# Kernel tuning notes

Hardware: AMD Instinct MI355X
Metric: run time of the kernel (lower is better)

Reference implementation:

```python
import jax, jax.numpy as jnp
import numpy as np

EPS = 1e-5

def _offset_conv(x, w, b):
    # 3x3 conv, padding=1, producing 2*K*K offset channels (standard DeformConv2D v1)
    out = jax.lax.conv_general_dilated(x, w, (1, 1), ((1, 1), (1, 1)),
                                       dimension_numbers=('NCHW', 'OIHW', 'NCHW'))
    return out + b[None, :, None, None]

def _bilinear_gather(x, py, px):
    # x: [B,C,H,W]; py,px: [B,K2,H,W] float sample coords -> [B,C,K2,H,W]
    B, C, H, W = x.shape
    py = jnp.clip(py, 0.0, H - 1.0)
    px = jnp.clip(px, 0.0, W - 1.0)
    y0 = jnp.floor(py)
    x0 = jnp.floor(px)
    wy = py - y0
    wx = px - x0
    y0i = y0.astype(jnp.int32)
    x0i = x0.astype(jnp.int32)
    y1i = jnp.minimum(y0i + 1, H - 1)
    x1i = jnp.minimum(x0i + 1, W - 1)
    xf = x.reshape(B, C, H * W)
    K2, Ho, Wo = py.shape[1], py.shape[2], py.shape[3]
    def gather(yy, xx):
        idx = (yy * W + xx).reshape(B, 1, -1)  # broadcast over C
        return jnp.take_along_axis(xf, idx, axis=2).reshape(B, C, K2, Ho, Wo)
    v00 = gather(y0i, x0i)
    v01 = gather(y0i, x1i)
    v10 = gather(y1i, x0i)
    v11 = gather(y1i, x1i)
    wy = wy[:, None]
    wx = wx[:, None]
    return (v00 * (1 - wy) * (1 - wx) + v01 * (1 - wy) * wx
            + v10 * wy * (1 - wx) + v11 * wy * wx)

def _deform_dw(x, w_off, b_off, w_dw, k):
    # depthwise deformable conv, kernel k, padding k//2 (same spatial size)
    B, C, H, W = x.shape
    K2 = k * k
    off = _offset_conv(x, w_off, b_off)      # [B, 2*K2, H, W]
    dy, dx = off[:, :K2], off[:, K2:]
    r = (k - 1) // 2
    pn = jnp.arange(-r, r + 1, dtype=x.dtype)
    pn_y = jnp.repeat(pn, k)[None, :, None, None]  # [1,K2,1,1]
    pn_x = jnp.tile(pn, k)[None, :, None, None]
    gy = jnp.arange(H, dtype=x.dtype)[None, None, :, None]
    gx = jnp.arange(W, dtype=x.dtype)[None, None, None, :]
    py = gy + pn_y + dy
    px = gx + pn_x + dx
    samp = _bilinear_gather(x, py, px)        # [B,C,K2,H,W]
    return jnp.einsum('bckhw,ck->bchw', samp, w_dw.reshape(C, K2))

def _bn_relu(x, g, b, m, v):
    inv = g / jnp.sqrt(v + EPS)
    return jax.nn.relu(x * inv[None, :, None, None] + (b - m * inv)[None, :, None, None])

def setup_inputs() -> dict:
    key = jax.random.key(0)
    B, C, H, W, O = 4, 96, 64, 64, 192
    ks = jax.random.split(key, 32)
    d = {'x': jax.random.normal(ks[0], (B, C, H, W), jnp.float32)}
    i = 1
    for k in (3, 5, 7):
        K2 = k * k
        d[f'w_off{k}'] = 0.01 * jax.random.normal(ks[i], (2 * K2, C, 3, 3), jnp.float32); i += 1
        d[f'b_off{k}'] = jnp.zeros((2 * K2,), jnp.float32)
        d[f'w_dw{k}'] = jax.random.normal(ks[i], (C, k, k), jnp.float32) / k; i += 1
        d[f'g{k}'] = jnp.ones((C,), jnp.float32)
        d[f'be{k}'] = jnp.zeros((C,), jnp.float32)
        d[f'm{k}'] = 0.1 * jax.random.normal(ks[i], (C,), jnp.float32); i += 1
        d[f'v{k}'] = jax.random.uniform(ks[i], (C,), jnp.float32, 0.5, 1.5); i += 1
    d['w_pw'] = jax.random.normal(ks[i], (O, 3 * C), jnp.float32) / np.sqrt(3 * C).astype(np.float32); i += 1
    d['gp'] = jnp.ones((O,), jnp.float32)
    d['bp'] = jnp.zeros((O,), jnp.float32)
    d['mp'] = 0.1 * jax.random.normal(ks[i], (O,), jnp.float32); i += 1
    d['vp'] = jax.random.uniform(ks[i], (O,), jnp.float32, 0.5, 1.5)
    return d

def reference(x, w_off3, b_off3, w_dw3, g3, be3, m3, v3,
              w_off5, b_off5, w_dw5, g5, be5, m5, v5,
              w_off7, b_off7, w_dw7, g7, be7, m7, v7,
              w_pw, gp, bp, mp, vp):
    x1 = _bn_relu(_deform_dw(x, w_off3, b_off3, w_dw3, 3), g3, be3, m3, v3)
    x2 = _bn_relu(_deform_dw(x, w_off5, b_off5, w_dw5, 5), g5, be5, m5, v5)
    x3 = _bn_relu(_deform_dw(x, w_off7, b_off7, w_dw7, 7), g7, be7, m7, v7)
    xc = jnp.concatenate([x1, x2, x3], axis=1)  # [B, 3C, H, W]
    out = jnp.einsum('bchw,oc->bohw', xc, w_pw)  # 1x1 conv
    return _bn_relu(out, gp, bp, mp, vp)
```

## Files before the change

### kernel.cpp

```cpp
#include <hip/hip_runtime.h>
#include <hip/hip_fp16.h>
#include <math.h>

typedef unsigned short u16;
typedef _Float16 f16x8 __attribute__((ext_vector_type(8)));
typedef float f32x4 __attribute__((ext_vector_type(4)));

#define HWp 4096
#define Cc 96
#define Bb 4
#define Oo 192
#define C3 288

#define OFF_WDWT  0
#define OFF_BCAT  14112
#define OFF_SBR   14304
#define OFF_HBR   14592
#define OFF_SPW   14880
#define OFF_HPW   15072
#define FP32_END  15264
#define BF_XTPAD  0
#define BF_WOF    1672704
#define BF_WPW    1838592

__device__ __forceinline__ u16 f2h(float f) { return __half_as_ushort(__float2half(f)); }
__device__ __forceinline__ unsigned h2u(__half2 h) { union { __half2 h; unsigned u; } t; t.h = h; return t.u; }
__device__ __forceinline__ __half2 u2h(unsigned u) { union { __half2 h; unsigned u; } t; t.u = u; return t.h; }

#define PREP_N (165888 + 55296 + 14112 + 192 + 288 + 288 + 192 + 192 + 24960)
#define PREP_BLK ((PREP_N + 255) / 256)

__global__ __launch_bounds__(256) void prep_kernel(
    const float* __restrict__ x,
    const float* __restrict__ w3, const float* __restrict__ b3, const float* __restrict__ dw3,
    const float* __restrict__ g3, const float* __restrict__ be3, const float* __restrict__ m3, const float* __restrict__ v3,
    const float* __restrict__ w5, const float* __restrict__ b5, const float* __restrict__ dw5,
    const float* __restrict__ g5, const float* __restrict__ be5, const float* __restrict__ m5, const float* __restrict__ v5,
    const float* __restrict__ w7, const float* __restrict__ b7, const float* __restrict__ dw7,
    const float* __restrict__ g7, const float* __restrict__ be7, const float* __restrict__ m7, const float* __restrict__ v7,
    const float* __restrict__ wpw,
    const float* __restrict__ gp, const float* __restrict__ bp, const float* __restrict__ mp, const float* __restrict__ vp,
    float* __restrict__ ws)
{
    __shared__ u16 sT[64 * 104];
    u16* bf = (u16*)(ws + FP32_END);
    const int tid = threadIdx.x;

    if (blockIdx.x < 256) {
        const int b = blockIdx.x >> 6, h = blockIdx.x & 63;
        const float* xb = x + (((size_t)b * Cc) << 12) + (h << 6);
#pragma unroll
        for (int it = 0; it < 24; ++it) {
            int j = tid + it * 256;
            int c = j >> 6, p = j & 63;
            sT[p * 104 + c] = f2h(xb[((size_t)c << 12) + p]);
        }
        __syncthreads();
        u16* dst = bf + BF_XTPAD + ((size_t)(b * 66 + h + 1) * 66 + 1) * 96;
#pragma unroll
        for (int it = 0; it < 6; ++it) {
            int j = tid + it * 256;
            int pos = j / 24, c4 = j % 24;
            const u16* s = &sT[pos * 104 + c4 * 4];
            *(uint2*)(dst + pos * 96 + c4 * 4) = make_uint2(
                (unsigned)s[0] | ((unsigned)s[1] << 16),
                (unsigned)s[2] | ((unsigned)s[3] << 16));
        }
        return;
    }

    int i = (blockIdx.x - 256) * 256 + tid;
    if (i < 165888) {
        int f = i / 13824, r = i % 13824;
        int s = r >> 9, l = r & 511;
        int lane = l >> 3, j = l & 7;
        int o = f * 16 + (lane & 15);
        int k = s * 32 + (lane >> 4) * 8 + j;
        int tap = k / 96, c = k % 96;
        float v = 0.f;
        if (o < 18)       v = w3[o * 864 + c * 9 + tap];
        else if (o < 68)  v = w5[(o - 18) * 864 + c * 9 + tap];
        else if (o < 166) v = w7[(o - 68) * 864 + c * 9 + tap];
        bf[BF_WOF + i] = f2h(v);
        return;
    }
    int j = i - 165888;
    if (j < 55296) {
        int f = j / 4608, r = j % 4608;
        int s = r >> 9, l = r & 511;
        int lane = l >> 3, jj = l & 7;
        int o = f * 16 + (lane & 15);
        int k = s * 32 + (lane >> 4) * 8 + jj;
        bf[BF_WPW + j] = f2h(wpw[o * C3 + k]);
        return;
    }
    j -= 55296;
    if (j < 14112) {
        int ksel = j / 4704, rem = j % 4704;
        int t = rem / 96, c = rem % 96;
        int K2 = (ksel == 0) ? 9 : (ksel == 1) ? 25 : 49;
        const float* dw = (ksel == 0) ? dw3 : (ksel == 1) ? dw5 : dw7;
        ws[OFF_WDWT + j] = (t < K2) ? dw[c * K2 + t] : 0.f;
        return;
    }
    j -= 14112;
    if (j < 192) {
        float v = 0.f;
        if (j < 18)       v = b3[j];
        else if (j < 68)  v = b5[j - 18];
        else if (j < 166) v = b7[j - 68];
        ws[OFF_BCAT + j] = v;
        return;
    }
    j -= 192;
    if (j < C3) {
        int ks = j / Cc, c = j % Cc;
        const float* g = (ks == 0) ? g3 : (ks == 1) ? g5 : g7;
        const float* v = (ks == 0) ? v3 : (ks == 1) ? v5 : v7;
        ws[OFF_SBR + j] = g[c] / sqrtf(v[c] + 1e-5f);
        return;
    }
    j -= C3;
    if (j < C3) {
        int ks = j / Cc, c = j % Cc;
        const float* g = (ks == 0) ? g3 : (ks == 1) ? g5 : g7;
        const float* v = (ks == 0) ? v3 : (ks == 1) ? v5 : v7;
        const float* be = (ks == 0) ? be3 : (ks == 1) ? be5 : be7;
        const float* m = (ks == 0) ? m3 : (ks == 1) ? m5 : m7;
        float inv = g[c] / sqrtf(v[c] + 1e-5f);
        ws[OFF_HBR + j] = be[c] - m[c] * inv;
        return;
    }
    j -= C3;
    if (j < Oo) { ws[OFF_SPW + j] = gp[j] / sqrtf(vp[j] + 1e-5f); return; }
    j -= Oo;
    if (j < Oo) {
        float inv = gp[j] / sqrtf(vp[j] + 1e-5f);
        ws[OFF_HPW + j] = bp[j] - mp[j] * inv;
        return;
    }
    j -= Oo;
    if (j < 24960) {
        int c4 = j % 24, rem = j / 24;
        int cell = rem % 260, bb = rem / 260;
        int row, col;
        if (cell < 66)       { row = 0;  col = cell; }
        else if (cell < 132) { row = 65; col = cell - 66; }
        else if (cell < 196) { row = cell - 132 + 1; col = 0; }
        else                 { row = cell - 196 + 1; col = 65; }
        u16* dst = bf + BF_XTPAD + ((size_t)(bb * 66 + row) * 66 + col) * 96 + c4 * 4;
        *(uint2*)dst = make_uint2(0u, 0u);
        return;
    }
}

__global__ __launch_bounds__(256, 4) void mega_kernel(
    const float* __restrict__ ws, float* __restrict__ out)
{
    __shared__ __align__(16) unsigned char shA[15936];
    __shared__ float regB[3072];
    u16* sX = (u16*)shA;
    uint2* sWab = (uint2*)shA;
    unsigned* sPk = (unsigned*)(shA + 10624);
    float* soff = regB;
    u16* ytile = (u16*)regB;

    const u16* bf = (const u16*)(ws + FP32_END);
    const u16* xp = bf + BF_XTPAD;
    const int tid = threadIdx.x;
    const int lane = tid & 63, wid = tid >> 6;
    const int lane15 = lane & 15, quad = lane >> 4;

    const int bx = blockIdx.x;
    const int xcd = bx & 7;
    const int b = xcd >> 1;
    const int tile = ((bx >> 3) << 1) + (xcd & 1);
    const int p0 = tile * 16;
    const int h = p0 >> 6;
    const int w0 = p0 & 63;

    {
        const u16* src = xp + ((size_t)(b * 66 + h) * 66 + w0) * 96;
        for (int j = tid; j < 1296; j += 256) {
            int r = j / 432;
            int rem = j % 432;
            int col = rem / 24, c4 = rem % 24;
            uint2 v = *(const uint2*)(src + ((size_t)(r * 66 + col)) * 96 + c4 * 4);
            *(uint2*)(&sX[(r * 18 + col) * 104 + c4 * 4]) = v;
        }
    }
    __syncthreads();

    {
        const u16* wof = bf + BF_WOF;
        f32x4 acc[3];
#pragma unroll
        for (int ff = 0; ff < 3; ++ff) acc[ff] = (f32x4){0.f, 0.f, 0.f, 0.f};
#pragma unroll
        for (int tap = 0; tap < 9; ++tap) {
            const int ky2 = tap / 3, kx2 = tap % 3;
            const u16* brow = &sX[(ky2 * 18 + kx2 + lane15) * 104 + quad * 8];
#pragma unroll
            for (int cc = 0; cc < 3; ++cc) {
                f16x8 bb = *(const f16x8*)(brow + cc * 32);
                const int s = tap * 3 + cc;
#pragma unroll
                for (int ff = 0; ff < 3; ++ff) {
                    const int f = wid * 3 + ff;
                    f16x8 a = *(const f16x8*)(wof + ((size_t)(f * 27 + s) * 64 + lane) * 8);
                    acc[ff] = __builtin_amdgcn_mfma_f32_16x16x32_f16(a, bb, acc[ff], 0, 0, 0);
                }
            }
        }
        const float* bcat = ws + OFF_BCAT;
#pragma unroll
        for (int ff = 0; ff < 3; ++ff) {
#pragma unroll
            for (int r = 0; r < 4; ++r) {
                int co = (wid * 3 + ff) * 16 + quad * 4 + r;
                soff[co * 16 + lane15] = acc[ff][r] + bcat[co];
            }
        }
    }
    __syncthreads();

    for (int i = tid; i < 1328; i += 256) {
        int gt = i >> 4, q = i & 15;
        int K, K2, R, tb, t;
        if (gt < 9)       { K = 3; K2 = 9;  R = 1; tb = 0;  t = gt; }
        else if (gt < 34) { K = 5; K2 = 25; R = 2; tb = 18; t = gt - 9; }
        else              { K = 7; K2 = 49; R = 3; tb = 68; t = gt - 34; }
        int ky = t / K - R, kx = t % K - R;
        float dy = soff[(tb + t) * 16 + q];
        float dx = soff[(tb + K2 + t) * 16 + q];
        float py = fminf(fmaxf((float)(h + ky) + dy, 0.f), 63.f);
        float px = fminf(fmaxf((float)(w0 + q + kx) + dx, 0.f), 63.f);
        float fy = floorf(py), fx = floorf(px);
        int y0 = (int)fy, x0 = (int)fx;
        float wy = py - fy, wx = px - fx;
        int y1 = min(y0 + 1, 63), x1 = min(x0 + 1, 63);
        float w11 = wy * wx;
        float w10 = wy - w11;
        float w01 = wx - w11;
        float w00 = 1.f - wy - wx + w11;
        unsigned wA = h2u(__floats2half2_rn(w00, w01));
        unsigned wB = h2u(__floats2half2_rn(w10, w11));
        unsigned o00 = (unsigned)((y0 + 1) * 66 + (x0 + 1)) * 192u;
        sWab[i] = make_uint2(wA, wB);
        sPk[i] = o00 | ((unsigned)(x1 - x0) << 20) | ((unsigned)(y1 - y0) << 21);
    }
    __syncthreads();

    if (tid < 192) {
        const int c8 = tid % 12;
        const int q  = tid / 12;
        const int c = c8 * 8;
        const u16* xh = xp + (size_t)b * 66 * 66 * 96;
        const char* xcb = (const char*)xh + c * 2;

#pragma unroll
        for (int seg = 0; seg < 3; ++seg) {
            const int g0 = (seg == 0) ? 0 : (seg == 1) ? 9 : 34;
            const int g1 = (seg == 0) ? 9 : (seg == 1) ? 34 : 83;
            const float* wdT = ws + OFF_WDWT + seg * 4704 + c;
            float acc[8];
#pragma unroll
            for (int k = 0; k < 8; ++k) acc[k] = 0.f;

            for (int gt = g0; gt < g1; ++gt) {
                const uint2 wab = sWab[(gt << 4) + q];
                const unsigned pk = sPk[(gt << 4) + q];
                const __half2 wAh = u2h(wab.x), wBh = u2h(wab.y);
                const __half2 w00b = __low2half2(wAh), w01b = __high2half2(wAh);
                const __half2 w10b = __low2half2(wBh), w11b = __high2half2(wBh);
                const unsigned d01 = ((pk >> 20) & 1u) * 192u;
                const unsigned d10 = ((pk >> 21) & 1u) * 12672u;
                const char* pb = xcb + (pk & 0xFFFFFu);
                const uint4 u00 = *(const uint4*)(pb);
                const uint4 u01 = *(const uint4*)(pb + d01);
                const uint4 u10 = *(const uint4*)(pb + d10);
                const uint4 u11 = *(const uint4*)(pb + d10 + d01);
                const float4 wda = *(const float4*)(wdT + (gt - g0) * 96);
                const float4 wdb = *(const float4*)(wdT + (gt - g0) * 96 + 4);
                const unsigned a00[4] = {u00.x, u00.y, u00.z, u00.w};
                const unsigned a01[4] = {u01.x, u01.y, u01.z, u01.w};
                const unsigned a10[4] = {u10.x, u10.y, u10.z, u10.w};
                const unsigned a11[4] = {u11.x, u11.y, u11.z, u11.w};
                const float wd[8] = {wda.x, wda.y, wda.z, wda.w, wdb.x, wdb.y, wdb.z, wdb.w};
#pragma unroll
                for (int d = 0; d < 4; ++d) {
                    __half2 v = __hmul2(w00b, u2h(a00[d]));
                    v = __hfma2(w01b, u2h(a01[d]), v);
                    v = __hfma2(w10b, u2h(a10[d]), v);
                    v = __hfma2(w11b, u2h(a11[d]), v);
                    acc[2 * d]     = fmaf(wd[2 * d],     __low2float(v),  acc[2 * d]);
                    acc[2 * d + 1] = fmaf(wd[2 * d + 1], __high2float(v), acc[2 * d + 1]);
                }
            }

            const int cb = seg * Cc + c;
            const float4 sa = *(const float4*)(ws + OFF_SBR + cb);
            const float4 sb = *(const float4*)(ws + OFF_SBR + cb + 4);
            const float4 ha = *(const float4*)(ws + OFF_HBR + cb);
            const float4 hb = *(const float4*)(ws + OFF_HBR + cb + 4);
            const float ss[8] = {sa.x, sa.y, sa.z, sa.w, sb.x, sb.y, sb.z, sb.w};
            const float hh8[8] = {ha.x, ha.y, ha.z, ha.w, hb.x, hb.y, hb.z, hb.w};
            unsigned rr[4];
#pragma unroll
            for (int d = 0; d < 4; ++d) {
                float lo = fmaxf(fmaf(acc[2 * d],     ss[2 * d],     hh8[2 * d]),     0.f);
                float hi = fmaxf(fmaf(acc[2 * d + 1], ss[2 * d + 1], hh8[2 * d + 1]), 0.f);
                rr[d] = h2u(__floats2half2_rn(lo, hi));
            }
            *(uint4*)(ytile + q * 296 + cb) = make_uint4(rr[0], rr[1], rr[2], rr[3]);
        }
    }
    __syncthreads();

    {
        const u16* wpw = bf + BF_WPW;
        f32x4 acc[3];
#pragma unroll
        for (int ff = 0; ff < 3; ++ff) acc[ff] = (f32x4){0.f, 0.f, 0.f, 0.f};
        const u16* brow = &ytile[lane15 * 296 + quad * 8];
#pragma unroll
        for (int s = 0; s < 9; ++s) {
            f16x8 bb = *(const f16x8*)(brow + s * 32);
#pragma unroll
            for (int ff = 0; ff < 3; ++ff) {
                const int f = wid * 3 + ff;
                f16x8 a = *(const f16x8*)(wpw + ((size_t)(f * 9 + s) * 64 + lane) * 8);
                acc[ff] = __builtin_amdgcn_mfma_f32_16x16x32_f16(a, bb, acc[ff], 0, 0, 0);
            }
        }
        const float* spw = ws + OFF_SPW;
        const float* hpw = ws + OFF_HPW;
        const int p = p0 + lane15;
#pragma unroll
        for (int ff = 0; ff < 3; ++ff) {
#pragma unroll
            for (int r = 0; r < 4; ++r) {
                int o = (wid * 3 + ff) * 16 + quad * 4 + r;
                out[(((size_t)(b * Oo + o)) << 12) + p] =
                    fmaxf(fmaf(acc[ff][r], spw[o], hpw[o]), 0.f);
            }
        }
    }
}

extern "C" void kernel_launch(void* const* d_in, const int* in_sizes, int n_in,
                              void* d_out, int out_size, void* d_ws, size_t ws_size,
                              hipStream_t stream)
{
    const float* x     = (const float*)d_in[0];
    const float* w3    = (const float*)d_in[1];
    const float* b3    = (const float*)d_in[2];
    const float* dw3   = (const float*)d_in[3];
    const float* g3    = (const float*)d_in[4];
    const float* be3   = (const float*)d_in[5];
    const float* m3    = (const float*)d_in[6];
    const float* v3    = (const float*)d_in[7];
    const float* w5    = (const float*)d_in[8];
    const float* b5    = (const float*)d_in[9];
    const float* dw5   = (const float*)d_in[10];
    const float* g5    = (const float*)d_in[11];
    const float* be5   = (const float*)d_in[12];
    const float* m5    = (const float*)d_in[13];
    const float* v5    = (const float*)d_in[14];
    const float* w7    = (const float*)d_in[15];
    const float* b7    = (const float*)d_in[16];
    const float* dw7   = (const float*)d_in[17];
    const float* g7    = (const float*)d_in[18];
    const float* be7   = (const float*)d_in[19];
    const float* m7    = (const float*)d_in[20];
    const float* v7    = (const float*)d_in[21];
    const float* wpw   = (const float*)d_in[22];
    const float* gp    = (const float*)d_in[23];
    const float* bp    = (const float*)d_in[24];
    const float* mp    = (const float*)d_in[25];
    const float* vp    = (const float*)d_in[26];

    float* ws = (float*)d_ws;
    float* out = (float*)d_out;

    {
        prep_kernel<<<256 + PREP_BLK, 256, 0, stream>>>(
            x,
            w3, b3, dw3, g3, be3, m3, v3,
            w5, b5, dw5, g5, be5, m5, v5,
            w7, b7, dw7, g7, be7, m7, v7,
            wpw, gp, bp, mp, vp, ws);
    }
    {
        mega_kernel<<<1024, 256, 0, stream>>>(ws, out);
    }
}
```

Before: 174.6 us.

## Split 5x5 deformable taps across idle fourth wavefront and drop clamp bits

In the deformable sampling stage, the fourth wavefront (tid 192-255) previously sat idle. It now computes 17 of the 25 taps of the 5x5 branch for all 192 (pixel, channel-group) slots, three slots per thread. Those partials go through a new shared buffer and are added in after an extra barrier. The packed offset also loses its x1/y1 clamp bits and always reads neighbours at +192/+12672 bytes. This should be safe because the input is padded and the weight for the extra neighbour is zero. The change balances per-thread work at the cost of extra LDS use, another __syncthreads, and a possible drop in occupancy.

Result: slower. 219.8 us (+25.9%).

```diff
diff --git a/kernel.cpp b/kernel.cpp
--- a/kernel.cpp
+++ b/kernel.cpp
@@ -159,6 +159,7 @@
 {
     __shared__ __align__(16) unsigned char shA[15936];
     __shared__ float regB[3072];
+    __shared__ float sP1[1728];
     u16* sX = (u16*)shA;
     uint2* sWab = (uint2*)shA;
     unsigned* sPk = (unsigned*)(shA + 10624);
@@ -238,82 +239,113 @@
         float fy = floorf(py), fx = floorf(px);
         int y0 = (int)fy, x0 = (int)fx;
         float wy = py - fy, wx = px - fx;
-        int y1 = min(y0 + 1, 63), x1 = min(x0 + 1, 63);
         float w11 = wy * wx;
         float w10 = wy - w11;
         float w01 = wx - w11;
         float w00 = 1.f - wy - wx + w11;
-        unsigned wA = h2u(__floats2half2_rn(w00, w01));
-        unsigned wB = h2u(__floats2half2_rn(w10, w11));
-        unsigned o00 = (unsigned)((y0 + 1) * 66 + (x0 + 1)) * 192u;
-        sWab[i] = make_uint2(wA, wB);
-        sPk[i] = o00 | ((unsigned)(x1 - x0) << 20) | ((unsigned)(y1 - y0) << 21);
+        sWab[i] = make_uint2(h2u(__floats2half2_rn(w00, w01)),
+                             h2u(__floats2half2_rn(w10, w11)));
+        sPk[i] = (unsigned)((y0 + 1) * 66 + (x0 + 1)) * 192u;
     }
     __syncthreads();
+
+#define TAP8(ACC, GT, Q, XCB, WDP) { \
+    const uint2 wab = sWab[((GT) << 4) + (Q)]; \
+    const unsigned o00 = sPk[((GT) << 4) + (Q)]; \
+    const __half2 wAh = u2h(wab.x), wBh = u2h(wab.y); \
+    const __half2 w00b = __low2half2(wAh), w01b = __high2half2(wAh); \
+    const __half2 w10b = __low2half2(wBh), w11b = __high2half2(wBh); \
+    const char* pb = (XCB) + o00; \
+    const uint4 u00 = *(const uint4*)(pb); \
+    const uint4 u01 = *(const uint4*)(pb + 192); \
+    const uint4 u10 = *(const uint4*)(pb + 12672); \
+    const uint4 u11 = *(const uint4*)(pb + 12864); \
+    const float4 wda = *(const float4*)(WDP); \
+    const float4 wdb = *(const float4*)((WDP) + 4); \
+    const unsigned a00[4] = {u00.x, u00.y, u00.z, u00.w}; \
+    const unsigned a01[4] = {u01.x, u01.y, u01.z, u01.w}; \
+    const unsigned a10[4] = {u10.x, u10.y, u10.z, u10.w}; \
+    const unsigned a11[4] = {u11.x, u11.y, u11.z, u11.w}; \
+    const float wd8[8] = {wda.x, wda.y, wda.z, wda.w, wdb.x, wdb.y, wdb.z, wdb.w}; \
+    _Pragma("unroll") \
+    for (int d = 0; d < 4; ++d) { \
+        __half2 v = __hmul2(w00b, u2h(a00[d])); \
+        v = __hfma2(w01b, u2h(a01[d]), v); \
+        v = __hfma2(w10b, u2h(a10[d]), v); \
+        v = __hfma2(w11b, u2h(a11[d]), v); \
+        ACC[2 * d]     = fmaf(wd8[2 * d],     __low2float(v),  ACC[2 * d]); \
+        ACC[2 * d + 1] = fmaf(wd8[2 * d + 1], __high2float(v), ACC[2 * d + 1]); \
+    } }
+
+#define BN_STORE(ACC, CB, Q) { \
+    const float4 sa = *(const float4*)(ws + OFF_SBR + (CB)); \
+    const float4 sb = *(const float4*)(ws + OFF_SBR + (CB) + 4); \
+    const float4 ha = *(const float4*)(ws + OFF_HBR + (CB)); \
+    const float4 hb = *(const float4*)(ws + OFF_HBR + (CB) + 4); \
+    const float ss8[8] = {sa.x, sa.y, sa.z, sa.w, sb.x, sb.y, sb.z, sb.w}; \
+    const float hh8[8] = {ha.x, ha.y, ha.z, ha.w, hb.x, hb.y, hb.z, hb.w}; \
+    unsigned rr[4]; \
+    _Pragma("unroll") \
+    for (int d = 0; d < 4; ++d) { \
+        float lo = fmaxf(fmaf(ACC[2 * d],     ss8[2 * d],     hh8[2 * d]),     0.f); \
+        float hi = fmaxf(fmaf(ACC[2 * d + 1], ss8[2 * d + 1], hh8[2 * d + 1]), 0.f); \
+        rr[d] = h2u(__floats2half2_rn(lo, hi)); \
+    } \
+    *(uint4*)(ytile + (Q) * 296 + (CB)) = make_uint4(rr[0], rr[1], rr[2], rr[3]); }
+
+    float acc1[8] = {0.f, 0.f, 0.f, 0.f, 0.f, 0.f, 0.f, 0.f};
+    const u16* xh = xp + (size_t)b * 66 * 66 * 96;
 
     if (tid < 192) {
         const int c8 = tid % 12;
         const int q  = tid / 12;
         const int c = c8 * 8;
-        const u16* xh = xp + (size_t)b * 66 * 66 * 96;
         const char* xcb = (const char*)xh + c * 2;
 
-#pragma unroll
-        for (int seg = 0; seg < 3; ++seg) {
-            const int g0 = (seg == 0) ? 0 : (seg == 1) ? 9 : 34;
-            const int g1 = (seg == 0) ? 9 : (seg == 1) ? 34 : 83;
-            const float* wdT = ws + OFF_WDWT + seg * 4704 + c;
-            float acc[8];
-#pragma unroll
-            for (int k = 0; k < 8; ++k) acc[k] = 0.f;
-
-            for (int gt = g0; gt < g1; ++gt) {
-                const uint2 wab = sWab[(gt << 4) + q];
-                const unsigned pk = sPk[(gt << 4) + q];
-                const __half2 wAh = u2h(wab.x), wBh = u2h(wab.y);
-                const __half2 w00b = __low2half2(wAh), w01b = __high2half2(wAh);
-                const __half2 w10b = __low2half2(wBh), w11b = __high2half2(wBh);
-                const unsigned d01 = ((pk >> 20) & 1u) * 192u;
-                const unsigned d10 = ((pk >> 21) & 1u) * 12672u;
-                const char* pb = xcb + (pk & 0xFFFFFu);
-                const uint4 u00 = *(const uint4*)(pb);
-                const uint4 u01 = *(const uint4*)(pb + d01);
-                const uint4 u10 = *(const uint4*)(pb + d10);
-                const uint4 u11 = *(const uint4*)(pb + d10 + d01);
-                const float4 wda = *(const float4*)(wdT + (gt - g0) * 96);
-                const float4 wdb = *(const float4*)(wdT + (gt - g0) * 96 + 4);
-                const unsigned a00[4] = {u00.x, u00.y, u00.z, u00.w};
-                const unsigned a01[4] = {u01.x, u01.y, u01.z, u01.w};
-                const unsigned a10[4] = {u10.x, u10.y, u10.z, u10.w};
-                const unsigned a11[4] = {u11.x, u11.y, u11.z, u11.w};
-                const float wd[8] = {wda.x, wda.y, wda.z, wda.w, wdb.x, wdb.y, wdb.z, wdb.w};
-#pragma unroll
-                for (int d = 0; d < 4; ++d) {
-                    __half2 v = __hmul2(w00b, u2h(a00[d]));
-                    v = __hfma2(w01b, u2h(a01[d]), v);
-                    v = __hfma2(w10b, u2h(a10[d]), v);
-                    v = __hfma2(w11b, u2h(a11[d]), v);
-                    acc[2 * d]     = fmaf(wd[2 * d],     __low2float(v),  acc[2 * d]);
-                    acc[2 * d + 1] = fmaf(wd[2 * d + 1], __high2float(v), acc[2 * d + 1]);
-                }
-            }
-
-            const int cb = seg * Cc + c;
-            const float4 sa = *(const float4*)(ws + OFF_SBR + cb);
-            const float4 sb = *(const float4*)(ws + OFF_SBR + cb + 4);
-            const float4 ha = *(const float4*)(ws + OFF_HBR + cb);
-            const float4 hb = *(const float4*)(ws + OFF_HBR + cb + 4);
-            const float ss[8] = {sa.x, sa.y, sa.z, sa.w, sb.x, sb.y, sb.z, sb.w};
-            const float hh8[8] = {ha.x, ha.y, ha.z, ha.w, hb.x, hb.y, hb.z, hb.w};
-            unsigned rr[4];
-#pragma unroll
-            for (int d = 0; d < 4; ++d) {
-                float lo = fmaxf(fmaf(acc[2 * d],     ss[2 * d],     hh8[2 * d]),     0.f);
-                float hi = fmaxf(fmaf(acc[2 * d + 1], ss[2 * d + 1], hh8[2 * d + 1]), 0.f);
-                rr[d] = h2u(__floats2half2_rn(lo, hi));
-            }
-            *(uint4*)(ytile + q * 296 + cb) = make_uint4(rr[0], rr[1], rr[2], rr[3]);
-        }
+        {
+            float acc[8] = {0.f, 0.f, 0.f, 0.f, 0.f, 0.f, 0.f, 0.f};
+            const float* wdT = ws + OFF_WDWT + c;
+            for (int gt = 0; gt < 9; ++gt)
+                TAP8(acc, gt, q, xcb, wdT + gt * 96);
+            BN_STORE(acc, c, q);
+        }
+        {
+            const float* wdT = ws + OFF_WDWT + 4704 + c;
+            for (int gt = 9; gt < 17; ++gt)
+                TAP8(acc1, gt, q, xcb, wdT + (gt - 9) * 96);
+        }
+        {
+            float acc[8] = {0.f, 0.f, 0.f, 0.f, 0.f, 0.f, 0.f, 0.f};
+            const float* wdT = ws + OFF_WDWT + 9408 + c;
+            for (int gt = 34; gt < 83; ++gt)
+                TAP8(acc, gt, q, xcb, wdT + (gt - 34) * 96);
+            BN_STORE(acc, 192 + c, q);
+        }
+    } else {
+        const int s = tid - 192;
+#pragma unroll
+        for (int k = 0; k < 3; ++k) {
+            const int slot = 3 * s + k;
+            const int q2 = slot / 12;
+            const int c2 = (slot % 12) * 8;
+            const char* xcb2 = (const char*)xh + c2 * 2;
+            const float* wdT = ws + OFF_WDWT + 4704 + c2;
+            float acc[8] = {0.f, 0.f, 0.f, 0.f, 0.f, 0.f, 0.f, 0.f};
+            for (int gt = 17; gt < 34; ++gt)
+                TAP8(acc, gt, q2, xcb2, wdT + (gt - 9) * 96);
+#pragma unroll
+            for (int jj = 0; jj < 8; ++jj) sP1[slot * 9 + jj] = acc[jj];
+        }
+    }
+    __syncthreads();
+
+    if (tid < 192) {
+        const int c8 = tid % 12;
+        const int q  = tid / 12;
+        const int c = c8 * 8;
+#pragma unroll
+        for (int jj = 0; jj < 8; ++jj) acc1[jj] += sP1[tid * 9 + jj];
+        BN_STORE(acc1, 96 + c, q);
     }
     __syncthreads();
 
```
